# Kernel optimization log

Measured on AMD Instinct MI355X. Metric: run time of the kernel, lower is better.

Reference implementation:

```python
import jax, jax.numpy as jnp
import numpy as np

B, T, W, HP = 1, 64, 88, 48   # batch, frames, pitches, hidden_per_pitch
NU, NH, K = 24, 4, 25          # n_unit, n_heads, neighborhood window
HD = NU // NH                  # head dim = 6
HL = NU // 2                   # LSTM hidden per direction = 12


def _lstm_bidir(x, w_ih, w_hh, b_ih, b_hh):
    # x: [N, T, In]; w_ih: [2, 4*HL, In]; w_hh: [2, 4*HL, HL]; biases: [2, 4*HL]
    N = x.shape[0]
    def run(Wih, Whh, bih, bhh, reverse):
        def step(carry, xt):
            h, c = carry
            g = xt @ Wih.T + h @ Whh.T + bih + bhh
            i, f, gg, o = jnp.split(g, 4, axis=-1)  # torch gate order i,f,g,o
            c = jax.nn.sigmoid(f) * c + jax.nn.sigmoid(i) * jnp.tanh(gg)
            h = jax.nn.sigmoid(o) * jnp.tanh(c)
            return (h, c), h
        init = (jnp.zeros((N, HL), x.dtype), jnp.zeros((N, HL), x.dtype))
        _, ys = jax.lax.scan(step, init, jnp.swapaxes(x, 0, 1), reverse=reverse)
        return jnp.swapaxes(ys, 0, 1)
    return jnp.concatenate([run(w_ih[0], w_hh[0], b_ih[0], b_hh[0], False),
                            run(w_ih[1], w_hh[1], b_ih[1], b_hh[1], True)], axis=-1)


def _natten2d(x, qkv_w, qkv_b, rpb, proj_w, proj_b):
    # Neighborhood attention over 2D grid [B, Hh, Ww] with KxK window clamped at borders.
    Bn, Hh, Ww, C = x.shape
    qkv = (x @ qkv_w.T + qkv_b).reshape(Bn, Hh, Ww, 3, NH, HD)
    q = qkv[..., 0, :, :] * (HD ** -0.5)
    k = qkv[..., 1, :, :]
    v = qkv[..., 2, :, :]
    half = K // 2
    ar = jnp.arange(K)
    idx_i = jnp.clip(jnp.arange(Hh) - half, 0, Hh - K)[:, None] + ar  # [Hh,K]
    idx_j = jnp.clip(jnp.arange(Ww) - half, 0, Ww - K)[:, None] + ar  # [Ww,K]
    kg = k[:, idx_i][:, :, :, idx_j]  # [B,Hh,K,Ww,K,NH,HD]
    vg = v[:, idx_i][:, :, :, idx_j]
    ri = idx_i - jnp.arange(Hh)[:, None] + (K - 1)  # relative pos bias indices [Hh,K]
    rj = idx_j - jnp.arange(Ww)[:, None] + (K - 1)  # [Ww,K]
    bias = rpb[:, ri][:, :, :, rj]                  # [NH,Hh,K,Ww,K]
    logits = jnp.einsum('bijnd,biajcnd->bnijac', q, kg)
    logits = logits + jnp.transpose(bias, (0, 1, 3, 2, 4))[None]
    attn = jax.nn.softmax(logits.reshape(Bn, NH, Hh, Ww, K * K), axis=-1)
    attn = attn.reshape(Bn, NH, Hh, Ww, K, K)
    out = jnp.einsum('bnijac,biajcnd->bijnd', attn, vg).reshape(Bn, Hh, Ww, C)
    return out @ proj_w.T + proj_b


def _forward(features, condition, mask, emb, w_ih_l0, w_hh_l0, b_ih_l0, b_hh_l0,
             w_ih_l1, w_hh_l1, b_ih_l1, b_hh_l1, qkv_w, qkv_b, rpb, proj_w, proj_b,
             out_w, out_b):
    # concat: [B,T,88,HP] + [B,T,88,4] + [B,T,88,1] -> [B,T,88,HP+5]
    cat = jnp.concatenate([jnp.transpose(features, (0, 1, 3, 2)), emb[condition],
                           mask[..., None]], axis=-1)
    x = jnp.transpose(cat, (0, 2, 1, 3)).reshape(B * W, T, HP + 5)  # pitchwise LSTM
    x = _lstm_bidir(x, w_ih_l0, w_hh_l0, b_ih_l0, b_hh_l0)
    x = _lstm_bidir(x, w_ih_l1, w_hh_l1, b_ih_l1, b_hh_l1)
    x = jnp.transpose(x.reshape(B, W, T, NU), (0, 2, 1, 3))  # [B,T,88,NU]
    for _ in range(2):  # n_layers=2; Sequential(*[m]*2) => SHARED weights
        x = _natten2d(x, qkv_w, qkv_b, rpb, proj_w, proj_b)
    return x @ out_w.T + out_b  # [B,T,88,5]


def setup_inputs():
    ks = jax.random.split(jax.random.key(0), 24)
    def unif(k, shape, fan):
        s = 1.0 / np.sqrt(fan)
        return jax.random.uniform(k, shape, jnp.float32, -s, s)
    return {
        'features': jax.random.normal(ks[0], (B, T, HP, W), jnp.float32),
        'condition': jax.random.randint(ks[1], (B, T, W), 0, 5),
        'mask': jax.random.uniform(ks[2], (B, T, W), jnp.float32),
        'emb': jax.random.normal(ks[3], (5, 4), jnp.float32),
        'w_ih_l0': unif(ks[4], (2, 4 * HL, HP + 5), HL),
        'w_hh_l0': unif(ks[5], (2, 4 * HL, HL), HL),
        'b_ih_l0': unif(ks[6], (2, 4 * HL), HL),
        'b_hh_l0': unif(ks[7], (2, 4 * HL), HL),
        'w_ih_l1': unif(ks[8], (2, 4 * HL, 2 * HL), HL),
        'w_hh_l1': unif(ks[9], (2, 4 * HL, HL), HL),
        'b_ih_l1': unif(ks[10], (2, 4 * HL), HL),
        'b_hh_l1': unif(ks[11], (2, 4 * HL), HL),
        'qkv_w': unif(ks[12], (3 * NU, NU), NU),
        'qkv_b': unif(ks[13], (3 * NU,), NU),
        'rpb': jax.random.normal(ks[14], (NH, 2 * K - 1, 2 * K - 1), jnp.float32) * 0.02,
        'proj_w': unif(ks[15], (NU, NU), NU),
        'proj_b': unif(ks[16], (NU,), NU),
        'out_w': unif(ks[17], (5, NU), NU),
        'out_b': unif(ks[18], (5,), NU),
    }


def reference(features, condition, mask, emb, w_ih_l0, w_hh_l0, b_ih_l0, b_hh_l0,
              w_ih_l1, w_hh_l1, b_ih_l1, b_hh_l1, qkv_w, qkv_b, rpb, proj_w, proj_b,
              out_w, out_b):
    return _forward(features, condition, mask, emb, w_ih_l0, w_hh_l0, b_ih_l0, b_hh_l0,
                    w_ih_l1, w_hh_l1, b_ih_l1, b_hh_l1, qkv_w, qkv_b, rpb,
                    proj_w, proj_b, out_w, out_b)
```

## Files before the change

### kernel.cpp

```cpp
#include <hip/hip_runtime.h>
#include <hip/hip_bf16.h>

#define NPIX (64*88)
#define NSEQ 88
#define TT 64
#define F0 53
#define GATES 48

typedef __hip_bfloat16 bf16;

__device__ __forceinline__ float frcp(float x){ return __builtin_amdgcn_rcpf(x); }
__device__ __forceinline__ float blo(unsigned u){ return __uint_as_float(u<<16); }
__device__ __forceinline__ float bhi(unsigned u){ return __uint_as_float(u & 0xffff0000u); }

__device__ __forceinline__ void unpack6(uint4 r, float* f){
  f[0] = __uint_as_float(r.x << 16);
  f[1] = __uint_as_float(r.x & 0xffff0000u);
  f[2] = __uint_as_float(r.y << 16);
  f[3] = __uint_as_float(r.y & 0xffff0000u);
  f[4] = __uint_as_float(r.z << 16);
  f[5] = __uint_as_float(r.z & 0xffff0000u);
}

__global__ __launch_bounds__(1024) void k_core(
    const float* __restrict__ feat, const int* __restrict__ cond,
    const float* __restrict__ mask, const float* __restrict__ emb,
    const float* __restrict__ wih0, const float* __restrict__ whh0,
    const float* __restrict__ bih0, const float* __restrict__ bhh0,
    const float* __restrict__ wih1, const float* __restrict__ whh1,
    const float* __restrict__ bih1, const float* __restrict__ bhh1,
    const float* __restrict__ qkv_w, const float* __restrict__ qkv_b,
    float* __restrict__ q, bf16* __restrict__ kh, bf16* __restrict__ vh){
  int n = (blockIdx.x & 7)*11 + (blockIdx.x >> 3);
  int tid = threadIdx.x;
  int wave = tid >> 6; int lane = tid & 63;
  __shared__ float smem[14816];
  float* gbuf = smem;
  float* sx   = smem + 6144;
  float* sw0  = smem + 6144+3392;
  float* w1   = smem + 6144;
  float* sqkv = smem + 6144+2400;
  float* y0   = smem + 6144+4200;
  float* y1   = smem + 6144+5736;
  float* bsum = smem + 14624;

  for (int idx = tid; idx < 2*GATES*F0; idx += 1024) sw0[idx] = wih0[idx];
  for (int idx = tid; idx < TT*F0; idx += 1024){
    int t = idx / F0, f = idx - t*F0;
    float v;
    if (f < 48)      v = feat[(t*48 + f)*88 + n];
    else if (f < 52) v = emb[cond[t*88+n]*4 + (f-48)];
    else             v = mask[t*88+n];
    sx[idx] = v;
  }
  if (tid < 96)       bsum[tid] = bih0[tid] + bhh0[tid];
  else if (tid < 192) bsum[tid] = bih1[tid-96] + bhh1[tid-96];
  __syncthreads();

  #pragma unroll
  for (int r = 0; r < 6; ++r){
    int row = tid + r*1024;
    int d = row / 3072; int rem = row - d*3072;
    int t = rem / 48; int j = rem - t*48;
    const float* xr = sx + t*F0;
    const float* wr = sw0 + (d*GATES + j)*F0;
    float a0=0.f, a1=0.f, a2=0.f, a3=0.f;
    #pragma unroll
    for (int f=0; f<52; f+=4){
      a0 += xr[f  ]*wr[f  ];
      a1 += xr[f+1]*wr[f+1];
      a2 += xr[f+2]*wr[f+2];
      a3 += xr[f+3]*wr[f+3];
    }
    gbuf[(d*TT + t)*GATES + j] = bsum[d*GATES+j] + xr[52]*wr[52] + ((a0+a1)+(a2+a3));
  }
  __syncthreads();

  if (wave >= 2){
    for (int idx = tid-128; idx < 2*GATES*24; idx += 896){
      int row = idx / 24, f = idx - row*24;
      w1[row*25 + f] = wih1[idx];
    }
    for (int idx = tid-128; idx < 72*24; idx += 896){
      int row = idx / 24, f = idx - row*24;
      sqkv[row*25 + f] = qkv_w[idx];
    }
  } else {
    int d = wave;
    int j = (lane < GATES) ? lane : (lane - GATES);
    int u = j % 12; int grp = j / 12;
    float w[12];
    const float* wb = whh0 + (d*GATES + j)*12;
    #pragma unroll
    for (int m=0;m<12;++m) w[m] = wb[m];
    float negs  = (grp==2) ? -2.f : -1.f;
    float amul  = (grp==2) ?  2.f :  1.f;
    float aadd  = (grp==2) ? -1.f :  0.f;
    const float* gb = gbuf + d*TT*GATES + j;
    float hval = 0.f, cval = 0.f;
    int t0 = d ? (TT-1) : 0;
    float gnext = gb[t0*GATES];
    for (int s=0;s<TT;++s){
      int t = d ? (TT-1-s) : s;
      float gg = gnext;
      int tn = d ? max(TT-2-s,0) : min(s+1,TT-1);
      gnext = gb[tn*GATES];
      float h0=__shfl(hval,0), h1=__shfl(hval,1), h2=__shfl(hval,2);
      float h3=__shfl(hval,3), h4=__shfl(hval,4), h5=__shfl(hval,5);
      float h6=__shfl(hval,6), h7=__shfl(hval,7), h8=__shfl(hval,8);
      float h9=__shfl(hval,9), h10=__shfl(hval,10), h11=__shfl(hval,11);
      float a0 = gg + h0*w[0] + h4*w[4] + h8*w[8];
      float a1 = h1*w[1] + h5*w[5] + h9*w[9];
      float a2 = h2*w[2] + h6*w[6] + h10*w[10];
      float a3 = h3*w[3] + h7*w[7] + h11*w[11];
      float dot = (a0+a1)+(a2+a3);
      float act = amul*frcp(1.f + __expf(negs*dot)) + aadd;
      float ai = __shfl(act, u);
      float af = __shfl(act, u+12);
      float ag = __shfl(act, u+24);
      float ao = __shfl(act, u+36);
      float cn = af*cval + ai*ag;
      float th = 2.f*frcp(1.f + __expf(-2.f*cn)) - 1.f;
      hval = ao*th; cval = cn;
      if (lane < 12) y0[t*24 + d*12 + lane] = hval;
    }
  }
  __syncthreads();

  #pragma unroll
  for (int r = 0; r < 6; ++r){
    int row = tid + r*1024;
    int d = row / 3072; int rem = row - d*3072;
    int t = rem / 48; int j = rem - t*48;
    const float* xr = y0 + t*24;
    const float* wr = w1 + (d*GATES + j)*25;
    float a0=0.f, a1=0.f;
    #pragma unroll
    for (int c=0; c<24; c+=2){ a0 += xr[c]*wr[c]; a1 += xr[c+1]*wr[c+1]; }
    gbuf[(d*TT + t)*GATES + j] = bsum[96 + d*GATES+j] + a0 + a1;
  }
  __syncthreads();

  if (wave < 2){
    int d = wave;
    int j = (lane < GATES) ? lane : (lane - GATES);
    int u = j % 12; int grp = j / 12;
    float w[12];
    const float* wb = whh1 + (d*GATES + j)*12;
    #pragma unroll
    for (int m=0;m<12;++m) w[m] = wb[m];
    float negs  = (grp==2) ? -2.f : -1.f;
    float amul  = (grp==2) ?  2.f :  1.f;
    float aadd  = (grp==2) ? -1.f :  0.f;
    const float* gb = gbuf + d*TT*GATES + j;
    float hval = 0.f, cval = 0.f;
    int t0 = d ? (TT-1) : 0;
    float gnext = gb[t0*GATES];
    for (int s=0;s<TT;++s){
      int t = d ? (TT-1-s) : s;
      float gg = gnext;
      int tn = d ? max(TT-2-s,0) : min(s+1,TT-1);
      gnext = gb[tn*GATES];
      float h0=__shfl(hval,0), h1=__shfl(hval,1), h2=__shfl(hval,2);
      float h3=__shfl(hval,3), h4=__shfl(hval,4), h5=__shfl(hval,5);
      float h6=__shfl(hval,6), h7=__shfl(hval,7), h8=__shfl(hval,8);
      float h9=__shfl(hval,9), h10=__shfl(hval,10), h11=__shfl(hval,11);
      float a0 = gg + h0*w[0] + h4*w[4] + h8*w[8];
      float a1 = h1*w[1] + h5*w[5] + h9*w[9];
      float a2 = h2*w[2] + h6*w[6] + h10*w[10];
      float a3 = h3*w[3] + h7*w[7] + h11*w[11];
      float dot = (a0+a1)+(a2+a3);
      float act = amul*frcp(1.f + __expf(negs*dot)) + aadd;
      float ai = __shfl(act, u);
      float af = __shfl(act, u+12);
      float ag = __shfl(act, u+24);
      float ao = __shfl(act, u+36);
      float cn = af*cval + ai*ag;
      float th = 2.f*frcp(1.f + __expf(-2.f*cn)) - 1.f;
      hval = ao*th; cval = cn;
      if (lane < 12) y1[t*24 + d*12 + lane] = hval;
    }
  }
  __syncthreads();

  for (int idx = tid; idx < TT*72; idx += 1024){
    int gq = idx % 72; int t = idx / 72;
    int p = t*88 + n;
    const float* xr = y1 + t*24;
    const float* wr = sqkv + gq*25;
    float a0=0.f, a1=0.f;
    #pragma unroll
    for (int c=0; c<24; c+=2){ a0 += xr[c]*wr[c]; a1 += xr[c+1]*wr[c+1]; }
    float acc = qkv_b[gq] + a0 + a1;
    int s = gq/24, rem = gq - s*24;
    if (s==0) q[p*24+rem] = acc*0.4082482904638631f;
    else {
      int hh = rem/6, pos = rem - hh*6;
      bf16* dst = (s==1) ? kh : vh;
      dst[((size_t)hh*NPIX + p)*8 + pos] = __float2bfloat16(acc);
    }
  }
}

__global__ __launch_bounds__(256) void k_attn1(
    const float* __restrict__ q, const bf16* __restrict__ kh,
    const bf16* __restrict__ vh, const float* __restrict__ rpb,
    const float* __restrict__ pw, const float* __restrict__ pb,
    const float* __restrict__ qkv_w, const float* __restrict__ qkv_b,
    float* __restrict__ q2, bf16* __restrict__ kh2, bf16* __restrict__ vh2){
  int p = blockIdx.x; int tid = threadIdx.x;
  int h = tid >> 6; int lane = tid & 63;
  int i = p / 88, j = p - i*88;
  int si = min(max(i-12,0),39), sj = min(max(j-12,0),63);
  __shared__ float aorow[24];
  __shared__ float xrow[24];

  float qv[6];
  #pragma unroll
  for (int d=0; d<6; ++d) qv[d] = q[p*24 + h*6 + d];
  const uint4* kb = (const uint4*)(kh + (size_t)h*NPIX*8);
  const uint4* vb = (const uint4*)(vh + (size_t)h*NPIX*8);
  float lgv[10]; int roff[10];
  float lmax = -1e30f;
  #pragma unroll
  for (int it=0; it<10; ++it){
    int nb = lane + it*64;
    bool valid = nb < 625;
    int nbc = valid ? nb : 624;
    int a = nbc/25, cc = nbc - a*25;
    int gi = si + a, gj = sj + cc;
    int row = gi*88+gj;
    roff[it] = row;
    float kr[6];
    unpack6(kb[row], kr);
    float lg = qv[0]*kr[0]+qv[1]*kr[1]+qv[2]*kr[2]+qv[3]*kr[3]+qv[4]*kr[4]+qv[5]*kr[5];
    lg += rpb[(h*49 + (gi - i + 24))*49 + (gj - j + 24)];
    lg = valid ? lg : -1e30f;
    lgv[it] = lg;
    lmax = fmaxf(lmax, lg);
  }
  #pragma unroll
  for (int off=32; off; off>>=1) lmax = fmaxf(lmax, __shfl_xor(lmax, off));
  float lsum = 0.f;
  #pragma unroll
  for (int it=0; it<10; ++it){
    float pe = __expf(lgv[it]-lmax);
    lgv[it] = pe; lsum += pe;
  }
  #pragma unroll
  for (int off=32; off; off>>=1) lsum += __shfl_xor(lsum, off);
  float acc[6] = {0,0,0,0,0,0};
  #pragma unroll
  for (int it=0; it<10; ++it){
    float vr[6];
    unpack6(vb[roff[it]], vr);
    float pe = lgv[it];
    #pragma unroll
    for (int d=0; d<6; ++d) acc[d] += pe*vr[d];
  }
  #pragma unroll
  for (int d=0; d<6; ++d){
    #pragma unroll
    for (int off=32; off; off>>=1) acc[d] += __shfl_xor(acc[d], off);
  }
  if (lane == 0){
    float inv = frcp(lsum);
    #pragma unroll
    for (int d=0; d<6; ++d) aorow[h*6+d] = acc[d]*inv;
  }
  __syncthreads();

  if (tid < 24){
    float a2 = pb[tid];
    const float* wr = pw + tid*24;
    #pragma unroll
    for (int c=0;c<24;++c) a2 += aorow[c]*wr[c];
    xrow[tid] = a2;
  }
  __syncthreads();

  if (tid < 72){
    float a2 = qkv_b[tid];
    const float* wr = qkv_w + tid*24;
    #pragma unroll
    for (int c=0;c<24;++c) a2 += xrow[c]*wr[c];
    int s = tid/24, rem = tid - s*24;
    if (s==0) q2[p*24+rem] = a2*0.4082482904638631f;
    else {
      int hh = rem/6, pos = rem - hh*6;
      bf16* dst = (s==1) ? kh2 : vh2;
      dst[((size_t)hh*NPIX + p)*8 + pos] = __float2bfloat16(a2);
    }
  }
}

__global__ __launch_bounds__(512) void k_attn(
    const float* __restrict__ q, const bf16* __restrict__ kh,
    const bf16* __restrict__ vh, const float* __restrict__ rpb,
    float* __restrict__ ao){
  int b = blockIdx.x;
  int h = b / 704; int rem = b - h*704;
  int ti = rem / 44, tj = rem - ti*44;
  int i0 = ti*4, j0 = tj*2;
  int tid = threadIdx.x;
  int w = tid >> 6; int lane = tid & 63;
  int osi = min(max(i0-12,0),39);
  int osj = min(max(j0-12,0),63);

  __shared__ unsigned kt[728*5];
  __shared__ unsigned vt[728*5];
  const uint4* kg = (const uint4*)(kh + (size_t)h*NPIX*8);
  const uint4* vg = (const uint4*)(vh + (size_t)h*NPIX*8);
  for (int idx = tid; idx < 728; idx += 512){
    int a = idx / 26, cc = idx - a*26;
    int gi = min(osi + a, 63), gj = min(osj + cc, 87);
    int src = gi*88 + gj;
    uint4 kr = kg[src];
    uint4 vr = vg[src];
    int o = idx*5;
    kt[o] = kr.x; kt[o+1] = kr.y; kt[o+2] = kr.z;
    vt[o] = vr.x; vt[o+1] = vr.y; vt[o+2] = vr.z;
  }
  __syncthreads();

  int pi = i0 + (w>>1), pj = j0 + (w&1);
  int p = pi*88 + pj;
  int dsi = min(max(pi-12,0),39) - osi;
  int dsj = min(max(pj-12,0),63) - osj;
  int rbi = osi + dsi - pi + 24;
  int rbj = osj + dsj - pj + 24;

  float qv[6];
  #pragma unroll
  for (int d=0; d<6; ++d) qv[d] = q[p*24 + h*6 + d];

  float lgv[10]; int rof[10];
  float lmax = -1e30f;
  #pragma unroll
  for (int it=0; it<10; ++it){
    int nb = lane + it*64;
    bool valid = nb < 625;
    int nbc = valid ? nb : 624;
    int a = nbc/25, cc = nbc - a*25;
    int r5 = ((a+dsi)*26 + (cc+dsj))*5;
    rof[it] = r5;
    unsigned k0 = kt[r5], k1 = kt[r5+1], k2 = kt[r5+2];
    float lg = qv[0]*blo(k0)+qv[1]*bhi(k0)+qv[2]*blo(k1)
             + qv[3]*bhi(k1)+qv[4]*blo(k2)+qv[5]*bhi(k2);
    lg += rpb[(h*49 + (a + rbi))*49 + (cc + rbj)];
    lg = valid ? lg : -1e30f;
    lgv[it] = lg;
    lmax = fmaxf(lmax, lg);
  }
  #pragma unroll
  for (int off=32; off; off>>=1) lmax = fmaxf(lmax, __shfl_xor(lmax, off));
  float lsum = 0.f;
  #pragma unroll
  for (int it=0; it<10; ++it){
    float pe = __expf(lgv[it]-lmax);
    lgv[it] = pe; lsum += pe;
  }
  #pragma unroll
  for (int off=32; off; off>>=1) lsum += __shfl_xor(lsum, off);
  float acc[6] = {0,0,0,0,0,0};
  #pragma unroll
  for (int it=0; it<10; ++it){
    int r5 = rof[it];
    unsigned v0 = vt[r5], v1 = vt[r5+1], v2 = vt[r5+2];
    float pe = lgv[it];
    acc[0] += pe*blo(v0); acc[1] += pe*bhi(v0);
    acc[2] += pe*blo(v1); acc[3] += pe*bhi(v1);
    acc[4] += pe*blo(v2); acc[5] += pe*bhi(v2);
  }
  #pragma unroll
  for (int d=0; d<6; ++d){
    #pragma unroll
    for (int off=32; off; off>>=1) acc[d] += __shfl_xor(acc[d], off);
  }
  if (lane == 0){
    float inv = frcp(lsum);
    #pragma unroll
    for (int d=0; d<6; ++d) ao[p*24 + h*6 + d] = acc[d]*inv;
  }
}

__global__ __launch_bounds__(64) void k_proj_out(const float* __restrict__ ain,
    const float* __restrict__ pw, const float* __restrict__ pb,
    const float* __restrict__ ow, const float* __restrict__ ob,
    float* __restrict__ out){
  int p = blockIdx.x; int tid = threadIdx.x;
  __shared__ float arow[24];
  __shared__ float xrow[24];
  if (tid < 24) arow[tid] = ain[p*24+tid];
  __syncthreads();
  if (tid < 24){
    float a2 = pb[tid];
    const float* wr = pw + tid*24;
    #pragma unroll
    for (int c=0;c<24;++c) a2 += arow[c]*wr[c];
    xrow[tid] = a2;
  }
  __syncthreads();
  if (tid < 5){
    float a2 = ob[tid];
    const float* wr = ow + tid*24;
    #pragma unroll
    for (int c=0;c<24;++c) a2 += xrow[c]*wr[c];
    out[p*5+tid] = a2;
  }
}

extern "C" void kernel_launch(void* const* d_in, const int* in_sizes, int n_in,
                              void* d_out, int out_size, void* d_ws, size_t ws_size,
                              hipStream_t stream) {
  const float* feat    = (const float*)d_in[0];
  const int*   cond    = (const int*)  d_in[1];
  const float* mask    = (const float*)d_in[2];
  const float* emb     = (const float*)d_in[3];
  const float* w_ih_l0 = (const float*)d_in[4];
  const float* w_hh_l0 = (const float*)d_in[5];
  const float* b_ih_l0 = (const float*)d_in[6];
  const float* b_hh_l0 = (const float*)d_in[7];
  const float* w_ih_l1 = (const float*)d_in[8];
  const float* w_hh_l1 = (const float*)d_in[9];
  const float* b_ih_l1 = (const float*)d_in[10];
  const float* b_hh_l1 = (const float*)d_in[11];
  const float* qkv_w   = (const float*)d_in[12];
  const float* qkv_b   = (const float*)d_in[13];
  const float* rpb     = (const float*)d_in[14];
  const float* proj_w  = (const float*)d_in[15];
  const float* proj_b  = (const float*)d_in[16];
  const float* out_w   = (const float*)d_in[17];
  const float* out_b   = (const float*)d_in[18];
  float* out = (float*)d_out;

  float* ws  = (float*)d_ws;
  float* Q1  = ws;
  float* Q2  = Q1 + 135168;
  float* AO  = Q2 + 135168;
  bf16*  KH1 = (bf16*)(AO + 135168);
  bf16*  VH1 = KH1 + 180224;
  bf16*  KH2 = VH1 + 180224;
  bf16*  VH2 = KH2 + 180224;

  k_core<<<NSEQ, 1024, 0, stream>>>(
      feat, cond, mask, emb,
      w_ih_l0, w_hh_l0, b_ih_l0, b_hh_l0,
      w_ih_l1, w_hh_l1, b_ih_l1, b_hh_l1,
      qkv_w, qkv_b, Q1, KH1, VH1);

  k_attn1<<<NPIX, 256, 0, stream>>>(
      Q1, KH1, VH1, rpb, proj_w, proj_b, qkv_w, qkv_b,
      Q2, KH2, VH2);

  k_attn<<<4*16*44, 512, 0, stream>>>(Q2, KH2, VH2, rpb, AO);

  k_proj_out<<<NPIX, 64, 0, stream>>>(AO, proj_w, proj_b, out_w, out_b, out);
}
```

Before: 205.6 us.

## Restructure LSTM core with wave-uniform weight loads and DPP/readlane recurrence

The input-projection and QKV matmuls now assign each wave a wave-uniform group of six gate rows, with each lane handling one timestep. Weights are read straight from global memory as scalar loads instead of being staged in shared memory. The recurrent LSTM step swaps ds_bpermute shuffles for readlane broadcasts and quad DPP broadcasts, with gates interleaved four to a unit. It also pads the LDS layouts to 49, 25 and 73 strides to avoid bank conflicts and shrinks the shared footprint. The serial recurrence latency and weight-staging passes are the intended targets; the cost is more scalar loads and more registers per lane.

```diff
diff --git a/kernel.cpp b/kernel.cpp
--- a/kernel.cpp
+++ b/kernel.cpp
@@ -20,6 +20,56 @@
   f[3] = __uint_as_float(r.y & 0xffff0000u);
   f[4] = __uint_as_float(r.z << 16);
   f[5] = __uint_as_float(r.z & 0xffff0000u);
+}
+
+__device__ __forceinline__ float rl(float v, int l){
+  return __int_as_float(__builtin_amdgcn_readlane(__float_as_int(v), l));
+}
+template<int K> __device__ __forceinline__ float qbcast(float v){
+  constexpr int ctrl = K | (K<<2) | (K<<4) | (K<<6);
+  return __int_as_float(__builtin_amdgcn_update_dpp(0, __float_as_int(v), ctrl, 0xf, 0xf, true));
+}
+
+__device__ __forceinline__ void lstm_dir(const float* __restrict__ whh,
+    const float* gb_base, float* ybuf, int d, int lane){
+  int u = lane >> 2, grp = lane & 3;
+  int uc = (u < 12) ? u : 11;
+  int j = grp*12 + uc;
+  float w[12];
+  const float* wb = whh + (d*GATES + j)*12;
+  #pragma unroll
+  for (int m=0;m<12;++m) w[m] = wb[m];
+  float negs = (grp==2) ? -2.f : -1.f;
+  float amul = (grp==2) ?  2.f :  1.f;
+  float aadd = (grp==2) ? -1.f :  0.f;
+  const float* gb = gb_base + (d*TT)*49 + j;
+  float hval = 0.f, cval = 0.f;
+  int t0 = d ? (TT-1) : 0;
+  float gnext = gb[t0*49];
+  bool wr = (grp==0) && (u < 12);
+  for (int s=0;s<TT;++s){
+    int t = d ? (TT-1-s) : s;
+    float gg = gnext;
+    int tn = d ? max(TT-2-s,0) : min(s+1,TT-1);
+    gnext = gb[tn*49];
+    float h0=rl(hval,0),  h1=rl(hval,4),  h2=rl(hval,8),   h3=rl(hval,12);
+    float h4=rl(hval,16), h5=rl(hval,20), h6=rl(hval,24),  h7=rl(hval,28);
+    float h8=rl(hval,32), h9=rl(hval,36), h10=rl(hval,40), h11=rl(hval,44);
+    float a0 = gg + h0*w[0] + h4*w[4] + h8*w[8];
+    float a1 = h1*w[1] + h5*w[5] + h9*w[9];
+    float a2 = h2*w[2] + h6*w[6] + h10*w[10];
+    float a3 = h3*w[3] + h7*w[7] + h11*w[11];
+    float dot = (a0+a1)+(a2+a3);
+    float act = amul*frcp(1.f + __expf(negs*dot)) + aadd;
+    float ai = qbcast<0>(act);
+    float af = qbcast<1>(act);
+    float ag = qbcast<2>(act);
+    float ao = qbcast<3>(act);
+    float cn = af*cval + ai*ag;
+    float th = 2.f*frcp(1.f + __expf(-2.f*cn)) - 1.f;
+    hval = ao*th; cval = cn;
+    if (wr) ybuf[t*25 + d*12 + u] = hval;
+  }
 }
 
 __global__ __launch_bounds__(1024) void k_core(
@@ -34,17 +84,13 @@
   int n = (blockIdx.x & 7)*11 + (blockIdx.x >> 3);
   int tid = threadIdx.x;
   int wave = tid >> 6; int lane = tid & 63;
-  __shared__ float smem[14816];
+  __shared__ float smem[12864];
   float* gbuf = smem;
-  float* sx   = smem + 6144;
-  float* sw0  = smem + 6144+3392;
-  float* w1   = smem + 6144;
-  float* sqkv = smem + 6144+2400;
-  float* y0   = smem + 6144+4200;
-  float* y1   = smem + 6144+5736;
-  float* bsum = smem + 14624;
-
-  for (int idx = tid; idx < 2*GATES*F0; idx += 1024) sw0[idx] = wih0[idx];
+  float* sx   = smem + 6272;
+  float* y0   = smem + 6272+3392;
+  float* y1   = smem + 6272+4992;
+  float* outb = smem;
+
   for (int idx = tid; idx < TT*F0; idx += 1024){
     int t = idx / F0, f = idx - t*F0;
     float v;
@@ -53,145 +99,99 @@
     else             v = mask[t*88+n];
     sx[idx] = v;
   }
-  if (tid < 96)       bsum[tid] = bih0[tid] + bhh0[tid];
-  else if (tid < 192) bsum[tid] = bih1[tid-96] + bhh1[tid-96];
-  __syncthreads();
-
-  #pragma unroll
-  for (int r = 0; r < 6; ++r){
-    int row = tid + r*1024;
-    int d = row / 3072; int rem = row - d*3072;
-    int t = rem / 48; int j = rem - t*48;
-    const float* xr = sx + t*F0;
-    const float* wr = sw0 + (d*GATES + j)*F0;
-    float a0=0.f, a1=0.f, a2=0.f, a3=0.f;
-    #pragma unroll
-    for (int f=0; f<52; f+=4){
-      a0 += xr[f  ]*wr[f  ];
-      a1 += xr[f+1]*wr[f+1];
-      a2 += xr[f+2]*wr[f+2];
-      a3 += xr[f+3]*wr[f+3];
-    }
-    gbuf[(d*TT + t)*GATES + j] = bsum[d*GATES+j] + xr[52]*wr[52] + ((a0+a1)+(a2+a3));
-  }
-  __syncthreads();
-
-  if (wave >= 2){
-    for (int idx = tid-128; idx < 2*GATES*24; idx += 896){
-      int row = idx / 24, f = idx - row*24;
-      w1[row*25 + f] = wih1[idx];
-    }
-    for (int idx = tid-128; idx < 72*24; idx += 896){
-      int row = idx / 24, f = idx - row*24;
-      sqkv[row*25 + f] = qkv_w[idx];
-    }
-  } else {
-    int d = wave;
-    int j = (lane < GATES) ? lane : (lane - GATES);
-    int u = j % 12; int grp = j / 12;
-    float w[12];
-    const float* wb = whh0 + (d*GATES + j)*12;
-    #pragma unroll
-    for (int m=0;m<12;++m) w[m] = wb[m];
-    float negs  = (grp==2) ? -2.f : -1.f;
-    float amul  = (grp==2) ?  2.f :  1.f;
-    float aadd  = (grp==2) ? -1.f :  0.f;
-    const float* gb = gbuf + d*TT*GATES + j;
-    float hval = 0.f, cval = 0.f;
-    int t0 = d ? (TT-1) : 0;
-    float gnext = gb[t0*GATES];
-    for (int s=0;s<TT;++s){
-      int t = d ? (TT-1-s) : s;
-      float gg = gnext;
-      int tn = d ? max(TT-2-s,0) : min(s+1,TT-1);
-      gnext = gb[tn*GATES];
-      float h0=__shfl(hval,0), h1=__shfl(hval,1), h2=__shfl(hval,2);
-      float h3=__shfl(hval,3), h4=__shfl(hval,4), h5=__shfl(hval,5);
-      float h6=__shfl(hval,6), h7=__shfl(hval,7), h8=__shfl(hval,8);
-      float h9=__shfl(hval,9), h10=__shfl(hval,10), h11=__shfl(hval,11);
-      float a0 = gg + h0*w[0] + h4*w[4] + h8*w[8];
-      float a1 = h1*w[1] + h5*w[5] + h9*w[9];
-      float a2 = h2*w[2] + h6*w[6] + h10*w[10];
-      float a3 = h3*w[3] + h7*w[7] + h11*w[11];
-      float dot = (a0+a1)+(a2+a3);
-      float act = amul*frcp(1.f + __expf(negs*dot)) + aadd;
-      float ai = __shfl(act, u);
-      float af = __shfl(act, u+12);
-      float ag = __shfl(act, u+24);
-      float ao = __shfl(act, u+36);
-      float cn = af*cval + ai*ag;
-      float th = 2.f*frcp(1.f + __expf(-2.f*cn)) - 1.f;
-      hval = ao*th; cval = cn;
-      if (lane < 12) y0[t*24 + d*12 + lane] = hval;
-    }
-  }
-  __syncthreads();
-
-  #pragma unroll
-  for (int r = 0; r < 6; ++r){
-    int row = tid + r*1024;
-    int d = row / 3072; int rem = row - d*3072;
-    int t = rem / 48; int j = rem - t*48;
-    const float* xr = y0 + t*24;
-    const float* wr = w1 + (d*GATES + j)*25;
-    float a0=0.f, a1=0.f;
-    #pragma unroll
-    for (int c=0; c<24; c+=2){ a0 += xr[c]*wr[c]; a1 += xr[c+1]*wr[c+1]; }
-    gbuf[(d*TT + t)*GATES + j] = bsum[96 + d*GATES+j] + a0 + a1;
-  }
-  __syncthreads();
-
-  if (wave < 2){
-    int d = wave;
-    int j = (lane < GATES) ? lane : (lane - GATES);
-    int u = j % 12; int grp = j / 12;
-    float w[12];
-    const float* wb = whh1 + (d*GATES + j)*12;
-    #pragma unroll
-    for (int m=0;m<12;++m) w[m] = wb[m];
-    float negs  = (grp==2) ? -2.f : -1.f;
-    float amul  = (grp==2) ?  2.f :  1.f;
-    float aadd  = (grp==2) ? -1.f :  0.f;
-    const float* gb = gbuf + d*TT*GATES + j;
-    float hval = 0.f, cval = 0.f;
-    int t0 = d ? (TT-1) : 0;
-    float gnext = gb[t0*GATES];
-    for (int s=0;s<TT;++s){
-      int t = d ? (TT-1-s) : s;
-      float gg = gnext;
-      int tn = d ? max(TT-2-s,0) : min(s+1,TT-1);
-      gnext = gb[tn*GATES];
-      float h0=__shfl(hval,0), h1=__shfl(hval,1), h2=__shfl(hval,2);
-      float h3=__shfl(hval,3), h4=__shfl(hval,4), h5=__shfl(hval,5);
-      float h6=__shfl(hval,6), h7=__shfl(hval,7), h8=__shfl(hval,8);
-      float h9=__shfl(hval,9), h10=__shfl(hval,10), h11=__shfl(hval,11);
-      float a0 = gg + h0*w[0] + h4*w[4] + h8*w[8];
-      float a1 = h1*w[1] + h5*w[5] + h9*w[9];
-      float a2 = h2*w[2] + h6*w[6] + h10*w[10];
-      float a3 = h3*w[3] + h7*w[7] + h11*w[11];
-      float dot = (a0+a1)+(a2+a3);
-      float act = amul*frcp(1.f + __expf(negs*dot)) + aadd;
-      float ai = __shfl(act, u);
-      float af = __shfl(act, u+12);
-      float ag = __shfl(act, u+24);
-      float ao = __shfl(act, u+36);
-      float cn = af*cval + ai*ag;
-      float th = 2.f*frcp(1.f + __expf(-2.f*cn)) - 1.f;
-      hval = ao*th; cval = cn;
-      if (lane < 12) y1[t*24 + d*12 + lane] = hval;
-    }
+  __syncthreads();
+
+  {
+    int wu = __builtin_amdgcn_readfirstlane(wave);
+    int dd = wu >> 3, jg = wu & 7;
+    const float* w0 = wih0 + (dd*GATES + jg*6)*F0;
+    const float* xr = sx + lane*F0;
+    float a0[6], a1[6];
+    #pragma unroll
+    for (int k=0;k<6;++k){
+      int j = dd*GATES + jg*6 + k;
+      a0[k] = bih0[j] + bhh0[j];
+      a1[k] = 0.f;
+    }
+    for (int f=0; f<52; f+=2){
+      float x0 = xr[f], x1 = xr[f+1];
+      #pragma unroll
+      for (int k=0;k<6;++k){
+        a0[k] += x0*w0[k*F0+f];
+        a1[k] += x1*w0[k*F0+f+1];
+      }
+    }
+    {
+      float x0 = xr[52];
+      #pragma unroll
+      for (int k=0;k<6;++k) a0[k] += x0*w0[k*F0+52];
+    }
+    float* go = gbuf + (dd*TT + lane)*49 + jg*6;
+    #pragma unroll
+    for (int k=0;k<6;++k) go[k] = a0[k] + a1[k];
+  }
+  __syncthreads();
+
+  if (wave < 2) lstm_dir(whh0, gbuf, y0, wave, lane);
+  __syncthreads();
+
+  {
+    int wu = __builtin_amdgcn_readfirstlane(wave);
+    int dd = wu >> 3, jg = wu & 7;
+    const float* w1p = wih1 + (dd*GATES + jg*6)*24;
+    const float* xr = y0 + lane*25;
+    float a0[6], a1[6];
+    #pragma unroll
+    for (int k=0;k<6;++k){
+      int j = dd*GATES + jg*6 + k;
+      a0[k] = bih1[j] + bhh1[j];
+      a1[k] = 0.f;
+    }
+    #pragma unroll
+    for (int c=0; c<24; c+=2){
+      float x0 = xr[c], x1 = xr[c+1];
+      #pragma unroll
+      for (int k=0;k<6;++k){
+        a0[k] += x0*w1p[k*24+c];
+        a1[k] += x1*w1p[k*24+c+1];
+      }
+    }
+    float* go = gbuf + (dd*TT + lane)*49 + jg*6;
+    #pragma unroll
+    for (int k=0;k<6;++k) go[k] = a0[k] + a1[k];
+  }
+  __syncthreads();
+
+  if (wave < 2) lstm_dir(whh1, gbuf, y1, wave, lane);
+  __syncthreads();
+
+  if (wave < 12){
+    int wu = __builtin_amdgcn_readfirstlane(wave);
+    int g0 = wu*6;
+    const float* qw = qkv_w + g0*24;
+    const float* xr = y1 + lane*25;
+    float a0[6], a1[6];
+    #pragma unroll
+    for (int k=0;k<6;++k){ a0[k] = qkv_b[g0+k]; a1[k] = 0.f; }
+    #pragma unroll
+    for (int c=0; c<24; c+=2){
+      float x0 = xr[c], x1 = xr[c+1];
+      #pragma unroll
+      for (int k=0;k<6;++k){
+        a0[k] += x0*qw[k*24+c];
+        a1[k] += x1*qw[k*24+c+1];
+      }
+    }
+    float* oo = outb + lane*73 + g0;
+    #pragma unroll
+    for (int k=0;k<6;++k) oo[k] = a0[k] + a1[k];
   }
   __syncthreads();
 
   for (int idx = tid; idx < TT*72; idx += 1024){
     int gq = idx % 72; int t = idx / 72;
     int p = t*88 + n;
-    const float* xr = y1 + t*24;
-    const float* wr = sqkv + gq*25;
-    float a0=0.f, a1=0.f;
-    #pragma unroll
-    for (int c=0; c<24; c+=2){ a0 += xr[c]*wr[c]; a1 += xr[c+1]*wr[c+1]; }
-    float acc = qkv_b[gq] + a0 + a1;
+    float acc = outb[t*73 + gq];
     int s = gq/24, rem = gq - s*24;
     if (s==0) q[p*24+rem] = acc*0.4082482904638631f;
     else {
```

After: 190.2 us. 7.5% less time.
